# Kernel tuning notes

Measured on AMD Instinct MI355X. Metric: run time of the kernel, lower is better.

The kernel has to match this reference:

```python
import jax, jax.numpy as jnp
import numpy as np
from math import sqrt

D_MODEL = 1024
N_HEADS = 16
FF_MULT = 4
MAX_DIST = 512
LN_EPS = 1e-5


def layer_norm(x, g, b):
    mu = jnp.mean(x, axis=-1, keepdims=True)
    var = jnp.var(x, axis=-1, keepdims=True)
    return (x - mu) * jax.lax.rsqrt(var + LN_EPS) * g + b


def setup_inputs() -> dict:
    key = jax.random.key(0)
    ks = jax.random.split(key, 10)
    D, H, F = D_MODEL, N_HEADS, D_MODEL * FF_MULT
    s = 0.02
    return {
        "x": jax.random.normal(ks[0], (2, 2048, D), dtype=jnp.float32),
        "w_qkv": jax.random.normal(ks[1], (D, 3 * D), dtype=jnp.float32) * s,
        "b_qkv": jnp.zeros((3 * D,), jnp.float32),
        "w_out": jax.random.normal(ks[2], (D, D), dtype=jnp.float32) * s,
        "b_out": jnp.zeros((D,), jnp.float32),
        "rel_bias": jax.random.normal(ks[3], (2 * MAX_DIST + 1, H), dtype=jnp.float32) * s,
        "g1": jnp.ones((D,), jnp.float32),
        "beta1": jnp.zeros((D,), jnp.float32),
        "w1": jax.random.normal(ks[4], (D, F), dtype=jnp.float32) * s,
        "b1": jnp.zeros((F,), jnp.float32),
        "w2": jax.random.normal(ks[5], (F, D), dtype=jnp.float32) * s,
        "b2": jnp.zeros((D,), jnp.float32),
        "g2": jnp.ones((D,), jnp.float32),
        "beta2": jnp.zeros((D,), jnp.float32),
    }


def reference(x, w_qkv, b_qkv, w_out, b_out, rel_bias, g1, beta1, w1, b1, w2, b2, g2, beta2):
    B, T, D = x.shape
    H = N_HEADS
    hd = D // H
    qkv = x @ w_qkv + b_qkv                      # [B,T,3D]
    q, k, v = jnp.split(qkv, 3, axis=-1)
    # [B,H,T,hd]
    q = q.reshape(B, T, H, hd).transpose(0, 2, 1, 3)
    k = k.reshape(B, T, H, hd).transpose(0, 2, 1, 3)
    v = v.reshape(B, T, H, hd).transpose(0, 2, 1, 3)
    scores = jnp.einsum("bhqd,bhkd->bhqk", q, k) / sqrt(hd)
    # relative position bias: gather from table [2*max_dist+1, H]
    rel = jnp.clip(jnp.arange(T)[None, :] - jnp.arange(T)[:, None], -MAX_DIST, MAX_DIST) + MAX_DIST
    bias = rel_bias[rel].transpose(2, 0, 1)       # [H,T,T]
    attn = jax.nn.softmax(scores + bias[None], axis=-1)
    out = jnp.einsum("bhqk,bhkd->bhqd", attn, v).transpose(0, 2, 1, 3).reshape(B, T, D)
    out = out @ w_out + b_out                     # dropout inactive (eval)
    x2 = layer_norm(x + out, g1, beta1)
    ff = jax.nn.gelu(x2 @ w1 + b1, approximate=False) @ w2 + b2
    x3 = layer_norm(x2 + ff, g2, beta2)
    return (x3, attn)
```

## Files before the change

### kernel.cpp

```cpp
#include <hip/hip_runtime.h>
#include <hip/hip_bf16.h>
#include <cstdint>
#include <cstddef>

#define DEVFN static __device__ __forceinline__

typedef __attribute__((ext_vector_type(8))) short bf16x8;
typedef __attribute__((ext_vector_type(4))) float f32x4;

#define WAITVM(N) asm volatile("s_waitcnt vmcnt(" #N ")" ::: "memory")
#define WAITLGKM() asm volatile("s_waitcnt lgkmcnt(0)" ::: "memory")
#define BAR() __builtin_amdgcn_s_barrier()

DEVFN ushort f2bf(float f) {
  uint32_t u = __float_as_uint(f);
  return (ushort)((u + 0x7fffu + ((u >> 16) & 1u)) >> 16);
}
DEVFN float bf2f(ushort u) { return __uint_as_float((uint32_t)u << 16); }

DEVFN void gl_lds16(const void* g, void* l) {
  __builtin_amdgcn_global_load_lds(
      (const __attribute__((address_space(1))) void*)g,
      (__attribute__((address_space(3))) void*)l, 16, 0, 0);
}

DEVFN float wred_sum(float v) {
#pragma unroll
  for (int o = 32; o; o >>= 1) v += __shfl_xor(v, o);
  return v;
}


__global__ __launch_bounds__(256) void pack_bf16(const float* __restrict__ in,
                                                 ushort* __restrict__ out) {
  size_t i = ((size_t)blockIdx.x * 256 + threadIdx.x) * 4;
  float4 v = *(const float4*)&in[i];
  ushort4 u = make_ushort4(f2bf(v.x), f2bf(v.y), f2bf(v.z), f2bf(v.w));
  *(ushort4*)&out[i] = u;
}

__global__ __launch_bounds__(256) void wtrans(const float* __restrict__ in,
                                              ushort* __restrict__ out,
                                              int K, int N) {
  __shared__ float tile[32][33];
  int n0 = blockIdx.x * 32, k0 = blockIdx.y * 32;
  int tid = threadIdx.x;
#pragma unroll
  for (int i = 0; i < 4; ++i) {
    int idx = tid + i * 256;
    int r = idx >> 5, c = idx & 31;
    tile[r][c] = in[(size_t)(k0 + r) * N + n0 + c];
  }
  __syncthreads();
#pragma unroll
  for (int i = 0; i < 4; ++i) {
    int idx = tid + i * 256;
    int r = idx >> 5, c = idx & 31;
    out[(size_t)(n0 + r) * K + k0 + c] = f2bf(tile[c][r]);
  }
}

__global__ __launch_bounds__(256) void pack_vT(const ushort* __restrict__ qkv,
                                               ushort* __restrict__ vT) {
  __shared__ ushort tile[64][72];
  int bh = blockIdx.y, b = bh >> 4, h = bh & 15;
  int t0 = blockIdx.x * 64;
  int tid = threadIdx.x;
#pragma unroll
  for (int i = 0; i < 16; ++i) {
    int idx = tid + i * 256;
    int r = idx >> 6, c = idx & 63;
    tile[r][c] = qkv[(size_t)(b * 2048 + t0 + r) * 3072 + 2048 + h * 64 + c];
  }
  __syncthreads();
#pragma unroll
  for (int i = 0; i < 16; ++i) {
    int idx = tid + i * 256;
    int d = idx >> 6, t = idx & 63;
    vT[((size_t)bh * 64 + d) * 2048 + t0 + t] = tile[t][d];
  }
}


template <bool GELU, bool STF32, bool STBF16>
__global__ __launch_bounds__(256)
void gemm128(const ushort* __restrict__ A, int lda,
             const ushort* __restrict__ BT, int ldb,
             const float* __restrict__ bias,
             float* __restrict__ Cf, ushort* __restrict__ Cb, int ldc, int K) {
  __shared__ ushort lsa[128 * 64];
  __shared__ ushort lsb[128 * 64];
  const int tid = threadIdx.x;
  const int lane = tid & 63;
  const int wv = tid >> 6;
  const int wr = (wv >> 1) * 64, wc = (wv & 1) * 64;
  const ushort* Ab = A + (size_t)blockIdx.y * 128 * lda;
  const ushort* Bb = BT + (size_t)blockIdx.x * 128 * ldb;
  f32x4 acc[4][4] = {};
  int rowS[4], slotS[4];
#pragma unroll
  for (int i = 0; i < 4; ++i) {
    int idx = tid + i * 256;
    rowS[i] = idx >> 3;
    slotS[i] = (idx & 7) ^ (rowS[i] & 7);
  }
  for (int kt = 0; kt < K; kt += 64) {
    __syncthreads();
#pragma unroll
    for (int i = 0; i < 4; ++i) {
      gl_lds16(Ab + (size_t)rowS[i] * lda + kt + slotS[i] * 8, &lsa[(tid + i * 256) * 8]);
      gl_lds16(Bb + (size_t)rowS[i] * ldb + kt + slotS[i] * 8, &lsb[(tid + i * 256) * 8]);
    }
    asm volatile("s_waitcnt vmcnt(0)" ::: "memory");
    __syncthreads();
#pragma unroll
    for (int kk = 0; kk < 2; ++kk) {
      bf16x8 af[4], bfr[4];
      const int g = kk * 4 + (lane >> 4);
#pragma unroll
      for (int m = 0; m < 4; ++m) {
        int r = wr + m * 16 + (lane & 15);
        af[m] = *(const bf16x8*)&lsa[r * 64 + ((g ^ (r & 7)) * 8)];
      }
#pragma unroll
      for (int n = 0; n < 4; ++n) {
        int r = wc + n * 16 + (lane & 15);
        bfr[n] = *(const bf16x8*)&lsb[r * 64 + ((g ^ (r & 7)) * 8)];
      }
#pragma unroll
      for (int m = 0; m < 4; ++m)
#pragma unroll
        for (int n = 0; n < 4; ++n)
          acc[m][n] = __builtin_amdgcn_mfma_f32_16x16x32_bf16(af[m], bfr[n], acc[m][n], 0, 0, 0);
    }
  }
  const int rb = blockIdx.y * 128 + wr + ((lane >> 4) << 2);
  const int cb = blockIdx.x * 128 + wc + (lane & 15);
#pragma unroll
  for (int m = 0; m < 4; ++m)
#pragma unroll
    for (int n = 0; n < 4; ++n) {
      int col = cb + n * 16;
      float bv = bias[col];
#pragma unroll
      for (int i = 0; i < 4; ++i) {
        int row = rb + m * 16 + i;
        float v = acc[m][n][i] + bv;
        if (GELU) v = 0.5f * v * (1.0f + erff(v * 0.70710678f));
        if (STF32) Cf[(size_t)row * ldc + col] = v;
        if (STBF16) Cb[(size_t)row * ldc + col] = f2bf(v);
      }
    }
}


__global__ __launch_bounds__(256)
void attn_fused(const ushort* __restrict__ qkv, const ushort* __restrict__ vT,
                const float* __restrict__ rel_bias,
                float* __restrict__ attn, ushort* __restrict__ ctx) {
  __shared__ ushort lsq[128 * 64];
  __shared__ ushort lsk[2][64 * 64];
  __shared__ ushort lsv[2][64 * 64];
  __shared__ ushort lsp[128 * 64];
  __shared__ float biasl[1025];
  const int tid = threadIdx.x;
  const int lane = tid & 63;
  const int wv = tid >> 6;
  const int bh = blockIdx.y, b = bh >> 4, h = bh & 15;
  const int q0 = blockIdx.x * 128;
  const ushort* qp = qkv + (size_t)b * 2048 * 3072 + h * 64;
  const ushort* kp = qp + 1024;
  const ushort* vp = vT + (size_t)bh * 64 * 2048;
  float* attnb = attn + (size_t)bh * 2048 * 2048;

  for (int i = tid; i < 1025; i += 256) biasl[i] = rel_bias[i * 16 + h];

#pragma unroll
  for (int i = 0; i < 4; ++i) {
    int idx = tid + i * 256;
    int row = idx >> 3;
    int slot = (idx & 7) ^ (row & 7);
    gl_lds16(qp + (size_t)(q0 + row) * 3072 + slot * 8, &lsq[idx * 8]);
  }

  const int r0 = tid >> 3;
  const int sl0 = (tid & 7) ^ (r0 & 7);
  const int r1 = (tid + 256) >> 3;
  const int sl1 = ((tid + 256) & 7) ^ (r1 & 7);

  auto stageK = [&](int t, int buf) {
    gl_lds16(kp + (size_t)(t * 64 + r0) * 3072 + sl0 * 8, &lsk[buf][tid * 8]);
    gl_lds16(kp + (size_t)(t * 64 + r1) * 3072 + sl1 * 8, &lsk[buf][(tid + 256) * 8]);
  };
  auto stageV = [&](int t, int buf) {
    gl_lds16(vp + (size_t)r0 * 2048 + t * 64 + sl0 * 8, &lsv[buf][tid * 8]);
    gl_lds16(vp + (size_t)r1 * 2048 + t * 64 + sl1 * 8, &lsv[buf][(tid + 256) * 8]);
  };

  auto mfmaS = [&](int buf, f32x4 accs[2][4]) {
    __builtin_amdgcn_s_setprio(1);
#pragma unroll
    for (int kk = 0; kk < 2; ++kk) {
      const int g = kk * 4 + (lane >> 4);
      bf16x8 aq[2], bk[4];
#pragma unroll
      for (int m = 0; m < 2; ++m) {
        int r = wv * 32 + m * 16 + (lane & 15);
        aq[m] = *(const bf16x8*)&lsq[r * 64 + ((g ^ (r & 7)) * 8)];
      }
#pragma unroll
      for (int n = 0; n < 4; ++n) {
        int r = n * 16 + (lane & 15);
        bk[n] = *(const bf16x8*)&lsk[buf][r * 64 + ((g ^ (r & 7)) * 8)];
      }
#pragma unroll
      for (int m = 0; m < 2; ++m)
#pragma unroll
        for (int n = 0; n < 4; ++n)
          accs[m][n] = __builtin_amdgcn_mfma_f32_16x16x32_bf16(aq[m], bk[n], accs[m][n], 0, 0, 0);
    }
    __builtin_amdgcn_s_setprio(0);
  };

  float l_part[8];
#pragma unroll
  for (int j = 0; j < 8; ++j) l_part[j] = 0.0f;

  stageK(0, 0);
  for (int t = 0; t < 32; ++t) {
    if (t < 31) {
      stageK(t + 1, (t + 1) & 1);
      WAITVM(2);
    } else {
      WAITVM(0);
    }
    WAITLGKM();
    BAR();
    f32x4 accs[2][4] = {};
    mfmaS(t & 1, accs);
#pragma unroll
    for (int m = 0; m < 2; ++m)
#pragma unroll
      for (int n = 0; n < 4; ++n)
#pragma unroll
        for (int i = 0; i < 4; ++i) {
          int row = q0 + wv * 32 + m * 16 + ((lane >> 4) << 2) + i;
          int col = t * 64 + n * 16 + (lane & 15);
          int rel = col - row;
          rel = rel < -512 ? -512 : (rel > 512 ? 512 : rel);
          float s = accs[m][n][i] * 0.125f + biasl[rel + 512];
          l_part[m * 4 + i] += __expf(s);
        }
    BAR();
  }

  float inv_l[8];
#pragma unroll
  for (int j = 0; j < 8; ++j) {
    float l = l_part[j];
    l += __shfl_xor(l, 1);
    l += __shfl_xor(l, 2);
    l += __shfl_xor(l, 4);
    l += __shfl_xor(l, 8);
    inv_l[j] = 1.0f / l;
  }

  f32x4 acc_o[2][4] = {};
  stageK(0, 0);
  stageV(0, 0);
  for (int t = 0; t < 32; ++t) {
    if (t < 31) {
      stageK(t + 1, (t + 1) & 1);
      stageV(t + 1, (t + 1) & 1);
      WAITVM(4);
    } else {
      WAITVM(0);
    }
    BAR();
    f32x4 accs[2][4] = {};
    mfmaS(t & 1, accs);
#pragma unroll
    for (int m = 0; m < 2; ++m)
#pragma unroll
      for (int n = 0; n < 4; ++n)
#pragma unroll
        for (int i = 0; i < 4; ++i) {
          int rloc = wv * 32 + m * 16 + ((lane >> 4) << 2) + i;
          int col = n * 16 + (lane & 15);
          int rel = (t * 64 + col) - (q0 + rloc);
          rel = rel < -512 ? -512 : (rel > 512 ? 512 : rel);
          float s = accs[m][n][i] * 0.125f + biasl[rel + 512];
          float p = __expf(s) * inv_l[m * 4 + i];
          lsp[rloc * 64 + (((col >> 3) ^ (rloc & 7)) << 3) + (col & 7)] = f2bf(p);
        }
    WAITLGKM();
    BAR();
    __builtin_amdgcn_s_setprio(1);
#pragma unroll
    for (int kk = 0; kk < 2; ++kk) {
      const int g = kk * 4 + (lane >> 4);
      bf16x8 ap[2], bv2[4];
#pragma unroll
      for (int m = 0; m < 2; ++m) {
        int r = wv * 32 + m * 16 + (lane & 15);
        ap[m] = *(const bf16x8*)&lsp[r * 64 + ((g ^ (r & 7)) * 8)];
      }
#pragma unroll
      for (int n = 0; n < 4; ++n) {
        int r = n * 16 + (lane & 15);
        bv2[n] = *(const bf16x8*)&lsv[t & 1][r * 64 + ((g ^ (r & 7)) * 8)];
      }
#pragma unroll
      for (int m = 0; m < 2; ++m)
#pragma unroll
        for (int n = 0; n < 4; ++n)
          acc_o[m][n] = __builtin_amdgcn_mfma_f32_16x16x32_bf16(ap[m], bv2[n], acc_o[m][n], 0, 0, 0);
    }
    __builtin_amdgcn_s_setprio(0);
#pragma unroll
    for (int j = 0; j < 4; ++j) {
      int idx = tid + j * 256;
      int row = idx >> 3, g2 = idx & 7;
      bf16x8 pv8 = *(const bf16x8*)&lsp[row * 64 + ((g2 ^ (row & 7)) * 8)];
      float* dst = attnb + (size_t)(q0 + row) * 2048 + t * 64 + g2 * 8;
      float4 f0 = make_float4(bf2f((ushort)pv8[0]), bf2f((ushort)pv8[1]),
                              bf2f((ushort)pv8[2]), bf2f((ushort)pv8[3]));
      float4 f1 = make_float4(bf2f((ushort)pv8[4]), bf2f((ushort)pv8[5]),
                              bf2f((ushort)pv8[6]), bf2f((ushort)pv8[7]));
      *(float4*)dst = f0;
      *(float4*)(dst + 4) = f1;
    }
    BAR();
  }

#pragma unroll
  for (int m = 0; m < 2; ++m)
#pragma unroll
    for (int n = 0; n < 4; ++n) {
      int col = h * 64 + n * 16 + (lane & 15);
#pragma unroll
      for (int i = 0; i < 4; ++i) {
        int row = q0 + wv * 32 + m * 16 + ((lane >> 4) << 2) + i;
        ctx[(size_t)(b * 2048 + row) * 1024 + col] = f2bf(acc_o[m][n][i]);
      }
    }
}


__global__ __launch_bounds__(256)
void add_ln(const float* __restrict__ a, const float* __restrict__ r,
            const float* __restrict__ g, const float* __restrict__ be,
            float* __restrict__ outf, ushort* __restrict__ outb) {
  const int tid = threadIdx.x;
  const size_t base = (size_t)blockIdx.x * 1024 + tid * 4;
  float4 va = *(const float4*)&a[base];
  float4 vr = *(const float4*)&r[base];
  float x0 = va.x + vr.x, x1 = va.y + vr.y, x2 = va.z + vr.z, x3 = va.w + vr.w;
  float s = x0 + x1 + x2 + x3;
  float s2 = x0 * x0 + x1 * x1 + x2 * x2 + x3 * x3;
  s = wred_sum(s);
  s2 = wred_sum(s2);
  __shared__ float rs[4], rq[4];
  if ((tid & 63) == 0) { rs[tid >> 6] = s; rq[tid >> 6] = s2; }
  __syncthreads();
  s = rs[0] + rs[1] + rs[2] + rs[3];
  s2 = rq[0] + rq[1] + rq[2] + rq[3];
  const float mean = s * (1.0f / 1024.0f);
  const float var = s2 * (1.0f / 1024.0f) - mean * mean;
  const float sc = rsqrtf(var + 1e-5f);
  float4 vg = *(const float4*)&g[tid * 4];
  float4 vb = *(const float4*)&be[tid * 4];
  float y0 = (x0 - mean) * sc * vg.x + vb.x;
  float y1 = (x1 - mean) * sc * vg.y + vb.y;
  float y2 = (x2 - mean) * sc * vg.z + vb.z;
  float y3 = (x3 - mean) * sc * vg.w + vb.w;
  *(float4*)&outf[base] = make_float4(y0, y1, y2, y3);
  if (outb) {
    ushort4 u = make_ushort4(f2bf(y0), f2bf(y1), f2bf(y2), f2bf(y3));
    *(ushort4*)&outb[base] = u;
  }
}


extern "C" void kernel_launch(void* const* d_in, const int* in_sizes, int n_in,
                              void* d_out, int out_size, void* d_ws, size_t ws_size,
                              hipStream_t stream) {
  const float* x     = (const float*)d_in[0];
  const float* w_qkv = (const float*)d_in[1];
  const float* b_qkv = (const float*)d_in[2];
  const float* w_out = (const float*)d_in[3];
  const float* b_out = (const float*)d_in[4];
  const float* relb  = (const float*)d_in[5];
  const float* g1    = (const float*)d_in[6];
  const float* be1   = (const float*)d_in[7];
  const float* w1    = (const float*)d_in[8];
  const float* b1    = (const float*)d_in[9];
  const float* w2    = (const float*)d_in[10];
  const float* b2    = (const float*)d_in[11];
  const float* g2    = (const float*)d_in[12];
  const float* be2   = (const float*)d_in[13];

  float* x3o  = (float*)d_out;
  float* attn = x3o + (size_t)4194304;

  char* w = (char*)d_ws;
  size_t off = 0;
  auto alloc = [&](size_t bytes) {
    void* p = w + off;
    off += (bytes + 255) & ~(size_t)255;
    return p;
  };
  ushort* x_bf   = (ushort*)alloc(4096ull * 1024 * 2);
  ushort* wqkvT  = (ushort*)alloc(3072ull * 1024 * 2);
  ushort* woutT  = (ushort*)alloc(1024ull * 1024 * 2);
  ushort* w1T    = (ushort*)alloc(4096ull * 1024 * 2);
  ushort* w2T    = (ushort*)alloc(1024ull * 4096 * 2);
  ushort* qkv_bf = (ushort*)alloc(4096ull * 3072 * 2);
  ushort* vT     = (ushort*)alloc(32ull * 64 * 2048 * 2);
  ushort* ctx_bf = (ushort*)alloc(4096ull * 1024 * 2);
  float*  projf  = (float*)alloc(4096ull * 1024 * 4);
  float*  x2f    = (float*)alloc(4096ull * 1024 * 4);
  ushort* x2bf   = (ushort*)alloc(4096ull * 1024 * 2);
  ushort* ff1_bf = (ushort*)alloc(4096ull * 4096 * 2);
  float*  ff2f   = projf;

  pack_bf16<<<4096, 256, 0, stream>>>(x, x_bf);
  wtrans<<<dim3(96, 32), 256, 0, stream>>>(w_qkv, wqkvT, 1024, 3072);
  wtrans<<<dim3(32, 32), 256, 0, stream>>>(w_out, woutT, 1024, 1024);
  wtrans<<<dim3(128, 32), 256, 0, stream>>>(w1, w1T, 1024, 4096);
  wtrans<<<dim3(32, 128), 256, 0, stream>>>(w2, w2T, 4096, 1024);

  gemm128<false, false, true><<<dim3(24, 32), 256, 0, stream>>>(
      x_bf, 1024, wqkvT, 1024, b_qkv, nullptr, qkv_bf, 3072, 1024);
  pack_vT<<<dim3(32, 32), 256, 0, stream>>>(qkv_bf, vT);
  attn_fused<<<dim3(16, 32), 256, 0, stream>>>(qkv_bf, vT, relb, attn, ctx_bf);

  gemm128<false, true, false><<<dim3(8, 32), 256, 0, stream>>>(
      ctx_bf, 1024, woutT, 1024, b_out, projf, nullptr, 1024, 1024);
  add_ln<<<4096, 256, 0, stream>>>(x, projf, g1, be1, x2f, x2bf);
  gemm128<true, false, true><<<dim3(32, 32), 256, 0, stream>>>(
      x2bf, 1024, w1T, 1024, b1, nullptr, ff1_bf, 4096, 1024);
  gemm128<false, true, false><<<dim3(8, 32), 256, 0, stream>>>(
      ff1_bf, 4096, w2T, 4096, b2, ff2f, nullptr, 1024, 4096);
  add_ln<<<4096, 256, 0, stream>>>(x2f, ff2f, g2, be2, x3o, nullptr);
}
```

Baseline: 508.4 us.

## Write attention probs directly from registers and use exp2 with prescaled bias

Attention probabilities are now stored straight from registers in fp32 to global memory during the softmax pass, instead of being reread from LDS as bf16 and written with a separate loop and barrier. The exponent now uses a hardware exp2 with the scale and log2e folded into a single fma and a prescaled bias table. The vmcnt waits are retuned so the outstanding attention stores do not block the K/V loads, and the launch bounds request two blocks per CU. The direct stores use scattered 4-byte writes instead of coalesced float4 writes, which may hurt store efficiency. Output precision improves because the stored probabilities are no longer rounded to bf16.

```diff
diff --git a/kernel.cpp b/kernel.cpp
--- a/kernel.cpp
+++ b/kernel.cpp
@@ -11,6 +11,8 @@
 #define WAITVM(N) asm volatile("s_waitcnt vmcnt(" #N ")" ::: "memory")
 #define WAITLGKM() asm volatile("s_waitcnt lgkmcnt(0)" ::: "memory")
 #define BAR() __builtin_amdgcn_s_barrier()
+
+DEVFN float exp2f_fast(float x) { return __builtin_amdgcn_exp2f(x); }
 
 DEVFN ushort f2bf(float f) {
   uint32_t u = __float_as_uint(f);
@@ -154,7 +156,7 @@
 }
 
 
-__global__ __launch_bounds__(256)
+__global__ __launch_bounds__(256, 2)
 void attn_fused(const ushort* __restrict__ qkv, const ushort* __restrict__ vT,
                 const float* __restrict__ rel_bias,
                 float* __restrict__ attn, ushort* __restrict__ ctx) {
@@ -172,8 +174,9 @@
   const ushort* kp = qp + 1024;
   const ushort* vp = vT + (size_t)bh * 64 * 2048;
   float* attnb = attn + (size_t)bh * 2048 * 2048;
-
-  for (int i = tid; i < 1025; i += 256) biasl[i] = rel_bias[i * 16 + h];
+  const float C_SC = 0.18033688011f;
+
+  for (int i = tid; i < 1025; i += 256) biasl[i] = rel_bias[i * 16 + h] * 1.44269504f;
 
 #pragma unroll
   for (int i = 0; i < 4; ++i) {
@@ -222,6 +225,8 @@
     __builtin_amdgcn_s_setprio(0);
   };
 
+  WAITLGKM();
+
   float l_part[8];
 #pragma unroll
   for (int j = 0; j < 8; ++j) l_part[j] = 0.0f;
@@ -234,7 +239,6 @@
     } else {
       WAITVM(0);
     }
-    WAITLGKM();
     BAR();
     f32x4 accs[2][4] = {};
     mfmaS(t & 1, accs);
@@ -248,8 +252,7 @@
           int col = t * 64 + n * 16 + (lane & 15);
           int rel = col - row;
           rel = rel < -512 ? -512 : (rel > 512 ? 512 : rel);
-          float s = accs[m][n][i] * 0.125f + biasl[rel + 512];
-          l_part[m * 4 + i] += __expf(s);
+          l_part[m * 4 + i] += exp2f_fast(fmaf(accs[m][n][i], C_SC, biasl[rel + 512]));
         }
     BAR();
   }
@@ -272,10 +275,10 @@
     if (t < 31) {
       stageK(t + 1, (t + 1) & 1);
       stageV(t + 1, (t + 1) & 1);
-      WAITVM(4);
-    } else {
-      WAITVM(0);
-    }
+    }
+    if (t == 0) { WAITVM(4); }
+    else if (t < 31) { WAITVM(36); }
+    else { WAITVM(32); }
     BAR();
     f32x4 accs[2][4] = {};
     mfmaS(t & 1, accs);
@@ -289,9 +292,9 @@
           int col = n * 16 + (lane & 15);
           int rel = (t * 64 + col) - (q0 + rloc);
           rel = rel < -512 ? -512 : (rel > 512 ? 512 : rel);
-          float s = accs[m][n][i] * 0.125f + biasl[rel + 512];
-          float p = __expf(s) * inv_l[m * 4 + i];
+          float p = exp2f_fast(fmaf(accs[m][n][i], C_SC, biasl[rel + 512])) * inv_l[m * 4 + i];
           lsp[rloc * 64 + (((col >> 3) ^ (rloc & 7)) << 3) + (col & 7)] = f2bf(p);
+          attnb[(size_t)(q0 + rloc) * 2048 + t * 64 + col] = p;
         }
     WAITLGKM();
     BAR();
@@ -317,20 +320,6 @@
           acc_o[m][n] = __builtin_amdgcn_mfma_f32_16x16x32_bf16(ap[m], bv2[n], acc_o[m][n], 0, 0, 0);
     }
     __builtin_amdgcn_s_setprio(0);
-#pragma unroll
-    for (int j = 0; j < 4; ++j) {
-      int idx = tid + j * 256;
-      int row = idx >> 3, g2 = idx & 7;
-      bf16x8 pv8 = *(const bf16x8*)&lsp[row * 64 + ((g2 ^ (row & 7)) * 8)];
-      float* dst = attnb + (size_t)(q0 + row) * 2048 + t * 64 + g2 * 8;
-      float4 f0 = make_float4(bf2f((ushort)pv8[0]), bf2f((ushort)pv8[1]),
-                              bf2f((ushort)pv8[2]), bf2f((ushort)pv8[3]));
-      float4 f1 = make_float4(bf2f((ushort)pv8[4]), bf2f((ushort)pv8[5]),
-                              bf2f((ushort)pv8[6]), bf2f((ushort)pv8[7]));
-      *(float4*)dst = f0;
-      *(float4*)(dst + 4) = f1;
-    }
-    BAR();
   }
 
 #pragma unroll
```

Result: no change. 513.9 us (+1.1%).
